# Kernel tuning notes

Hardware: AMD Instinct MI355X
Metric: run time of the kernel (lower is better)

## Reference

```python
import jax, jax.numpy as jnp
import numpy as np

L = 40   # seq_length (sentence includes root; sent_length = L-1)
B = 16   # batch
V = 10000  # vocab
F = 512  # feature_size = 2*hidden (bidirectional)
H = 256  # classifier hidden
NEG = -jnp.inf


def _mlp(x, W1, b1, W2, b2):
    # Classifier / BinaryClassifier: Linear -> tanh -> Linear
    return jnp.tanh(x @ W1 + b1) @ W2 + b2


def setup_inputs() -> dict:
    key = jax.random.key(0)
    ks = jax.random.split(key, 10)
    s = 0.05
    return {
        "h": jax.random.normal(ks[0], (L, B, F), jnp.float32),
        "sentence": jax.random.randint(ks[1], (L, B), 0, V),
        "Wt1": jax.random.normal(ks[2], (2 * F, H), jnp.float32) * s,
        "bt1": jnp.zeros((H,), jnp.float32),
        "Wt2": jax.random.normal(ks[3], (H, 1), jnp.float32) * s,
        "bt2": jnp.zeros((1,), jnp.float32),
        "Ww1": jax.random.normal(ks[4], (2 * F, H), jnp.float32) * s,
        "bw1": jnp.zeros((H,), jnp.float32),
        "Ww2": jax.random.normal(ks[5], (H, V), jnp.float32) * s,
        "bw2": jnp.zeros((V,), jnp.float32),
    }


def reference(h, sentence, Wt1, bt1, Wt2, bt2, Ww1, bw1, Ww2, bw2):
    sent_length = L - 1
    # all ordered pairs i < j (forward enumeration order of batch_feature_selection)
    iu, ju = np.triu_indices(L, k=1)          # [P]
    feat = jnp.concatenate([h[iu], h[ju]], axis=-1)   # [P, B, 2F]

    t_logit = _mlp(feat, Wt1, bt1, Wt2, bt2)[..., 0]  # [P, B]
    sh = jax.nn.log_sigmoid(-t_logit)                 # shift log-prob
    re = jax.nn.log_sigmoid(t_logit)                  # reduce log-prob

    # word model log-softmax, gathered at target token sentence[j+1]
    wl = _mlp(feat, Ww1, bw1, Ww2, bw2)               # [P, B, V]
    ju1 = np.minimum(ju + 1, L - 1)                   # pairs with j = L-1 are unused
    tgt = sentence[ju1]                               # [P, B]
    gathered = jnp.take_along_axis(wl, tgt[..., None], axis=-1)[..., 0]
    wlp = gathered - jax.nn.logsumexp(wl, axis=-1)    # [P, B]

    # dense [L, L, B] tables (only i<j entries used)
    SHW = jnp.full((L, L, B), NEG, jnp.float32).at[iu, ju].set(sh + wlp)  # word_prob_list
    RE = jnp.full((L, L, B), NEG, jnp.float32).at[iu, ju].set(re)

    # init cell: stack_next=False -> word prob of sentence[1] from features (0,0)
    feat0 = jnp.concatenate([h[0], h[0]], axis=-1)    # [B, 2F]
    lp0 = jax.nn.log_softmax(_mlp(feat0, Ww1, bw1, Ww2, bw2), axis=-1)
    init = jnp.take_along_axis(lp0, sentence[1][:, None], axis=1)[:, 0]  # [B]

    T = jnp.full((L, L, B), NEG, jnp.float32)
    T = T.at[0, 1].set(init)
    T = T.at[jnp.arange(1, sent_length), jnp.arange(2, sent_length + 1)].set(0.0)

    # CKY-style DP over span widths; each width is vectorized over start i and split k
    for gap in range(2, sent_length + 1):
        n_i = sent_length + 1 - gap
        i_arr = np.arange(n_i)
        j_arr = i_arr + gap
        k = i_arr[:, None] + np.arange(1, gap)[None, :]   # [n_i, gap-1]
        scores = (T[i_arr[:, None], k] + T[k, j_arr[:, None]]
                  + SHW[i_arr[:, None], k] + RE[k, j_arr[:, None]])  # [n_i, gap-1, B]
        T = T.at[i_arr, j_arr].set(jax.nn.logsumexp(scores, axis=1))

    # stack_next=False -> final_score = 0
    return T[0, sent_length]
```

## Files before the change

### kernel.cpp

```cpp
#include <hip/hip_runtime.h>
#include <hip/hip_bf16.h>

#define L_SEQ 40
#define B_SZ  16
#define V_SZ  10000
#define V_PAD 10240
#define NPAIR 780
#define NROWP 784
#define M_ROWS (NROWP * B_SZ)

typedef __attribute__((ext_vector_type(4))) float f32x4;
typedef __attribute__((ext_vector_type(4))) int   i32x4;
typedef __attribute__((ext_vector_type(8))) int   i32x8;

#if __has_builtin(__builtin_amdgcn_cvt_pk_fp8_f32)
__device__ __forceinline__ unsigned int pack4_fp8(float x0, float x1, float x2, float x3) {
    int lo = __builtin_amdgcn_cvt_pk_fp8_f32(x0, x1, 0, false);
    int full = __builtin_amdgcn_cvt_pk_fp8_f32(x2, x3, lo, true);
    return (unsigned int)full;
}
#else
__device__ __forceinline__ unsigned char f2e4m3(float f) {
    unsigned u = __float_as_uint(f);
    unsigned s = (u >> 24) & 0x80u;
    if ((u & 0x7FFFFFFFu) == 0) return (unsigned char)s;
    int E = (int)((u >> 23) & 0xFF) - 127 + 7;
    unsigned m = u & 0x7FFFFFu;
    if (E >= 16) return (unsigned char)(s | 0x7E);
    if (E >= 1) {
        unsigned keep = m >> 20, rest = m & 0xFFFFFu;
        keep += (rest > 0x80000u) || (rest == 0x80000u && (keep & 1));
        if (keep == 8) { keep = 0; E++; if (E >= 16) return (unsigned char)(s | 0x7E); }
        return (unsigned char)(s | (E << 3) | keep);
    }
    int shift = 1 - E;
    if (shift > 10) return (unsigned char)s;
    unsigned full = 0x800000u | m;
    unsigned sh = 20 + shift;
    unsigned keep = full >> sh, rem = full & ((1u << sh) - 1), half = 1u << (sh - 1);
    keep += (rem > half) || (rem == half && (keep & 1));
    if (keep >= 8) return (unsigned char)(s | (1 << 3));
    return (unsigned char)(s | keep);
}
__device__ __forceinline__ unsigned int pack4_fp8(float x0, float x1, float x2, float x3) {
    return (unsigned int)f2e4m3(x0) | ((unsigned int)f2e4m3(x1) << 8)
         | ((unsigned int)f2e4m3(x2) << 16) | ((unsigned int)f2e4m3(x3) << 24);
}
#endif

#if __has_builtin(__builtin_amdgcn_exp2f)
__device__ __forceinline__ float exp2_hw(float x) { return __builtin_amdgcn_exp2f(x); }
#else
__device__ __forceinline__ float exp2_hw(float x) { return __expf(x * 0.6931471805599453f); }
#endif

#if __has_builtin(__builtin_amdgcn_rcpf)
__device__ __forceinline__ float rcp_hw(float x) { return __builtin_amdgcn_rcpf(x); }
#else
__device__ __forceinline__ float rcp_hw(float x) { return 1.0f / x; }
#endif

__device__ __forceinline__ float fast_tanh(float x) {
    float e = exp2_hw(x * 2.885390081777926814f);
    return fmaf(-2.0f, rcp_hw(e + 1.0f), 1.0f);
}


__global__ __launch_bounds__(256) void prep_kernel(
        const float* __restrict__ Ww2, float* __restrict__ WwT,
        unsigned char* __restrict__ WbT,
        const float* __restrict__ h, const float* __restrict__ Wt1,
        const float* __restrict__ Ww1, float* __restrict__ UV) {
    const int bx = blockIdx.x;
    const int t = threadIdx.x;
    __shared__ float smem[32 * 132];
    if (bx < 640) {
        float (*tile)[132] = (float (*)[132])smem;
        int v0 = (bx % 80) * 128;
        int k0 = (bx / 80) * 32;
        int tx4 = t & 31, ky = t >> 5;
        int v = v0 + tx4 * 4;
#pragma unroll
        for (int r = 0; r < 4; r++) {
            int k = k0 + ky + r * 8;
            float4 val = make_float4(0.f, 0.f, 0.f, 0.f);
            if (v < V_SZ) val = *(const float4*)(Ww2 + (size_t)k * V_SZ + v);
            *(float4*)(&tile[ky + r * 8][tx4 * 4]) = val;
        }
        __syncthreads();
        int kx4 = t & 7, vr8 = t >> 3;
#pragma unroll
        for (int pass = 0; pass < 4; pass++) {
            int vr = vr8 + pass * 32;
            float c0 = tile[kx4 * 4 + 0][vr];
            float c1 = tile[kx4 * 4 + 1][vr];
            float c2 = tile[kx4 * 4 + 2][vr];
            float c3 = tile[kx4 * 4 + 3][vr];
            float4 cv = make_float4(c0, c1, c2, c3);
            *(float4*)(WwT + (size_t)(v0 + vr) * 256 + k0 + kx4 * 4) = cv;
            ((unsigned int*)WbT)[(size_t)(v0 + vr) * 64 + (k0 >> 2) + kx4] =
                pack4_fp8(c0, c1, c2, c3);
        }
    } else {
        float* hs = smem;
        int ub = bx - 640;
        int which = ub / 80;
        int m0 = (ub % 80) * 8;
        const float4* src = (const float4*)(h + (size_t)m0 * 512);
        float4* dst4 = (float4*)hs;
#pragma unroll
        for (int v = 0; v < 4; v++) dst4[v * 256 + t] = src[v * 256 + t];
        __syncthreads();
        const float* W = ((which < 2) ? Wt1 : Ww1) + ((which & 1) ? 512 * 256 : 0);
        float acc[8] = {};
        for (int f = 0; f < 512; f += 4) {
            float w0 = W[(f + 0) * 256 + t];
            float w1 = W[(f + 1) * 256 + t];
            float w2 = W[(f + 2) * 256 + t];
            float w3 = W[(f + 3) * 256 + t];
#pragma unroll
            for (int r = 0; r < 8; r++) {
                float4 hv = *(const float4*)(hs + r * 512 + f);
                acc[r] += hv.x * w0 + hv.y * w1 + hv.z * w2 + hv.w * w3;
            }
        }
        float* dst = UV + ((size_t)which * 640 + m0) * 256;
#pragma unroll
        for (int r = 0; r < 8; r++) dst[r * 256 + t] = acc[r];
    }
}

__global__ void build_rows(const float* __restrict__ UV,
                           const int* __restrict__ sentence,
                           const float* __restrict__ bt1,
                           const float* __restrict__ bw1,
                           const float* __restrict__ Wt2,
                           const float* __restrict__ bt2,
                           const float* __restrict__ WwT,
                           const float* __restrict__ bw2,
                           unsigned char* __restrict__ X,
                           float* __restrict__ tlog,
                           float* __restrict__ glog) {
    int w = blockIdx.x * 4 + (threadIdx.x >> 6);
    int lane = threadIdx.x & 63;
    int p = w >> 4, b = w & 15;
    int i = 0, j = 0;
    if (p < NPAIR) {
        int rem = p, len = L_SEQ - 1;
        while (rem >= len) { rem -= len; len--; i++; }
        j = i + 1 + rem;
    }
    int j1 = (j + 1 < L_SEQ) ? j + 1 : L_SEQ - 1;
    int tgt = sentence[j1 * B_SZ + b];
    const float4 ut = ((const float4*)(UV + 0 * 640 * 256 + (i * B_SZ + b) * 256))[lane];
    const float4 vt = ((const float4*)(UV + 1 * 640 * 256 + (j * B_SZ + b) * 256))[lane];
    const float4 uw = ((const float4*)(UV + 2 * 640 * 256 + (i * B_SZ + b) * 256))[lane];
    const float4 vw = ((const float4*)(UV + 3 * 640 * 256 + (j * B_SZ + b) * 256))[lane];
    const float4 bt = ((const float4*)bt1)[lane];
    const float4 bw = ((const float4*)bw1)[lane];
    const float4 w2 = ((const float4*)Wt2)[lane];
    const float4 wc = ((const float4*)(WwT + (size_t)tgt * 256))[lane];
    float xt0 = fast_tanh(ut.x + vt.x + bt.x), xt1 = fast_tanh(ut.y + vt.y + bt.y);
    float xt2 = fast_tanh(ut.z + vt.z + bt.z), xt3 = fast_tanh(ut.w + vt.w + bt.w);
    float xw0 = fast_tanh(uw.x + vw.x + bw.x), xw1 = fast_tanh(uw.y + vw.y + bw.y);
    float xw2 = fast_tanh(uw.z + vw.z + bw.z), xw3 = fast_tanh(uw.w + vw.w + bw.w);
    ((unsigned int*)X)[w * 64 + lane] = pack4_fp8(xw0, xw1, xw2, xw3);
    float td = xt0 * w2.x + xt1 * w2.y + xt2 * w2.z + xt3 * w2.w;
    float gd = xw0 * wc.x + xw1 * wc.y + xw2 * wc.z + xw3 * wc.w;
#pragma unroll
    for (int off = 32; off >= 1; off >>= 1) {
        td += __shfl_xor(td, off);
        gd += __shfl_xor(gd, off);
    }
    if (lane == 0) {
        tlog[w] = td + bt2[0];
        glog[w] = gd + bw2[tgt];
    }
}

#define RDQ(BASE, Q, BR) \
    BR[0] = *(const i32x4*)((BASE) + offs[(Q)*4+0]); \
    BR[1] = *(const i32x4*)((BASE) + offs[(Q)*4+1]); \
    BR[2] = *(const i32x4*)((BASE) + offs[(Q)*4+2]); \
    BR[3] = *(const i32x4*)((BASE) + offs[(Q)*4+3]);

#define MFQ(Q, BR) { \
    i32x8 bv0_ = __builtin_shufflevector(BR[0], BR[1], 0,1,2,3,4,5,6,7); \
    acc[0][((Q)&1)*2] = __builtin_amdgcn_mfma_scale_f32_16x16x128_f8f6f4( \
        apan[0][(Q)>>1], bv0_, acc[0][((Q)&1)*2], 0,0, 0,0x7F7F7F7F, 0,0x7F7F7F7F); \
    acc[1][((Q)&1)*2] = __builtin_amdgcn_mfma_scale_f32_16x16x128_f8f6f4( \
        apan[1][(Q)>>1], bv0_, acc[1][((Q)&1)*2], 0,0, 0,0x7F7F7F7F, 0,0x7F7F7F7F); \
    i32x8 bv1_ = __builtin_shufflevector(BR[2], BR[3], 0,1,2,3,4,5,6,7); \
    acc[0][((Q)&1)*2+1] = __builtin_amdgcn_mfma_scale_f32_16x16x128_f8f6f4( \
        apan[0][(Q)>>1], bv1_, acc[0][((Q)&1)*2+1], 0,0, 0,0x7F7F7F7F, 0,0x7F7F7F7F); \
    acc[1][((Q)&1)*2+1] = __builtin_amdgcn_mfma_scale_f32_16x16x128_f8f6f4( \
        apan[1][(Q)>>1], bv1_, acc[1][((Q)&1)*2+1], 0,0, 0,0x7F7F7F7F, 0,0x7F7F7F7F); \
}

__global__ __launch_bounds__(512, 2) void big_gemm(
        const unsigned char* __restrict__ X,
        const unsigned char* __restrict__ WbT,
        const float* __restrict__ bw2,
        float* __restrict__ rowsum) {
    __shared__ unsigned char Bs[3][64 * 256];
    __shared__ float biasL[2048];
    const int t = threadIdx.x;
    const int wid = t >> 6, lane = t & 63;
    const int l15 = lane & 15, l4 = lane >> 4;
    const int g = blockIdx.x;
    const int row0 = blockIdx.y * 256 + wid * 32;
    const int NIT = 32;
    const float L2E = 1.44269504088896340736f;

#pragma unroll
    for (int k = 0; k < 4; k++) {
        int idx = k * 512 + t;
        int col = g * 2048 + idx;
        biasL[idx] = (col < V_SZ) ? bw2[col] * L2E : -__builtin_inff();
    }

    int offs[16];
#pragma unroll
    for (int q = 0; q < 4; q++) {
        int kb = q >> 1, np = q & 1;
#pragma unroll
        for (int nn = 0; nn < 2; nn++)
#pragma unroll
            for (int gg = 0; gg < 2; gg++) {
                int ni = np * 2 + nn;
                int cc = ni * 16 + l15;
                int gr = kb * 8 + l4 * 2 + gg;
                offs[q * 4 + nn * 2 + gg] = cc * 256 + ((gr ^ (cc & 15)) << 4);
            }
    }

    auto dmaB = [&](int buf, int it) {
        const unsigned char* Bg = WbT + (size_t)(g * 2048 + it * 64) * 256;
#pragma unroll
        for (int q = 0; q < 2; q++) {
            int off = (wid * 2 + q) * 1024;
            int F = off + lane * 16;
            int cc = F >> 8;
            int s = (F >> 4) & 15;
            int srcg = s ^ (cc & 15);
            __builtin_amdgcn_global_load_lds(
                (const __attribute__((address_space(1))) unsigned int*)(Bg + cc * 256 + (srcg << 4)),
                (__attribute__((address_space(3))) unsigned int*)(&Bs[buf][0] + off),
                16, 0, 0);
        }
    };

    dmaB(0, 0);
    i32x8 apan[2][2];
    {
        const unsigned char* Ag = X + (size_t)row0 * 256;
#pragma unroll
        for (int mi = 0; mi < 2; mi++)
#pragma unroll
            for (int kb = 0; kb < 2; kb++)
                apan[mi][kb] = *(const i32x8*)(Ag + (mi * 16 + l15) * 256 + kb * 128 + l4 * 32);
    }
    dmaB(1, 1);
    __syncthreads();

    i32x4 br0[4], br1[4];
    RDQ(&Bs[0][0], 0, br0);

    float PS[2][4] = {};
    int bc = 0, bp = 2;

#pragma unroll 1
    for (int it = 0; it < NIT; it++) {
        asm volatile("s_waitcnt vmcnt(0)" ::: "memory");
        __builtin_amdgcn_s_barrier();
        if (it + 2 < NIT) dmaB(bp, it + 2);
        const unsigned char* bufC = &Bs[bc][0];
        int bn = (bc == 2) ? 0 : bc + 1;
        const unsigned char* bufN = &Bs[bn][0];
        float bl[4];
#pragma unroll
        for (int ni = 0; ni < 4; ni++) bl[ni] = biasL[it * 64 + ni * 16 + l15];
        f32x4 acc[2][4] = {};
        __builtin_amdgcn_s_setprio(1);
        RDQ(bufC, 1, br1); MFQ(0, br0);
        RDQ(bufC, 2, br0); MFQ(1, br1);
        RDQ(bufC, 3, br1); MFQ(2, br0);
        if (it + 1 < NIT) { RDQ(bufN, 0, br0); }
        MFQ(3, br1);
        __builtin_amdgcn_s_setprio(0);
#pragma unroll
        for (int ni = 0; ni < 4; ni++) {
            float bL = bl[ni];
#pragma unroll
            for (int mi = 0; mi < 2; mi++)
#pragma unroll
                for (int r = 0; r < 4; r++)
                    PS[mi][r] += exp2_hw(fmaf(acc[mi][ni][r], L2E, bL));
        }
        bc = bn;
        bp = (bp == 2) ? 0 : bp + 1;
    }
#pragma unroll
    for (int mi = 0; mi < 2; mi++)
#pragma unroll
        for (int r = 0; r < 4; r++) {
            float v = PS[mi][r];
            v += __shfl_xor(v, 1); v += __shfl_xor(v, 2);
            v += __shfl_xor(v, 4); v += __shfl_xor(v, 8);
            if (l15 == 0)
                atomicAdd(&rowsum[row0 + mi * 16 + l4 * 4 + r], v);
        }
}

__global__ __launch_bounds__(1024) void dp_kernel(const float* __restrict__ tlog,
                          const float* __restrict__ glog,
                          const float* __restrict__ rowsum,
                          float* __restrict__ out) {
    __shared__ float Tl[1600], SHWl[1600], REl[1600];
    const int t = threadIdx.x;
    const int b = blockIdx.x;
    const float NEGINF = -__builtin_inff();
    for (int idx = t; idx < 1600; idx += 1024) {
        Tl[idx] = NEGINF; SHWl[idx] = NEGINF; REl[idx] = NEGINF;
    }
    __syncthreads();
    for (int p = t; p < NPAIR; p += 1024) {
        int i = 0, rem = p, len = L_SEQ - 1;
        while (rem >= len) { rem -= len; len--; i++; }
        int j = i + 1 + rem;
        int row = p * 16 + b;
        float tl = tlog[row];
        float re_v = (tl >= 0.f) ? -log1pf(__expf(-tl)) : (tl - log1pf(__expf(tl)));
        float sh_v = (tl <= 0.f) ? -log1pf(__expf(tl)) : (-tl - log1pf(__expf(-tl)));
        float wlp = glog[row] - __logf(rowsum[row]);
        SHWl[i * 40 + j] = sh_v + wlp;
        REl[i * 40 + j] = re_v;
    }
    if (t == 0) {
        int row = NPAIR * 16 + b;
        Tl[0 * 40 + 1] = glog[row] - __logf(rowsum[row]);
    }
    if (t >= 1 && t <= 38) Tl[t * 40 + t + 1] = 0.f;
    __syncthreads();
    const int tg = t >> 4, li = t & 15;
    for (int gap = 2; gap <= L_SEQ - 1; gap++) {
        int n_i = L_SEQ - gap;
        float m = NEGINF, s = 0.f;
        int i = tg, j = tg + gap;
        if (tg < n_i) {
            for (int k = i + 1 + li; k < j; k += 16) {
                float v = Tl[i * 40 + k] + Tl[k * 40 + j]
                        + SHWl[i * 40 + k] + REl[k * 40 + j];
                if (v > m) { s = s * __expf(m - v) + 1.f; m = v; }
                else s += __expf(v - m);
            }
        }
#pragma unroll
        for (int off = 1; off < 16; off <<= 1) {
            float mo = __shfl_xor(m, off), so = __shfl_xor(s, off);
            float M = fmaxf(m, mo);
            float sn = 0.f;
            if (m > NEGINF) sn += s * __expf(m - M);
            if (mo > NEGINF) sn += so * __expf(mo - M);
            m = M; s = sn;
        }
        if (tg < n_i && li == 0) Tl[i * 40 + j] = m + __logf(s);
        __syncthreads();
    }
    if (t == 0) out[b] = Tl[39];
}

extern "C" void kernel_launch(void* const* d_in, const int* in_sizes, int n_in,
                              void* d_out, int out_size, void* d_ws, size_t ws_size,
                              hipStream_t stream) {
    const float* h        = (const float*)d_in[0];
    const int*   sentence = (const int*)d_in[1];
    const float* Wt1      = (const float*)d_in[2];
    const float* bt1      = (const float*)d_in[3];
    const float* Wt2      = (const float*)d_in[4];
    const float* bt2      = (const float*)d_in[5];
    const float* Ww1      = (const float*)d_in[6];
    const float* bw1      = (const float*)d_in[7];
    const float* Ww2      = (const float*)d_in[8];
    const float* bw2      = (const float*)d_in[9];
    float* out = (float*)d_out;

    char* ws = (char*)d_ws;
    size_t off = 0;
    float* UV = (float*)(ws + off);                    off += 4ull * 640 * 256 * 4;
    unsigned char* X = (unsigned char*)(ws + off);     off += (size_t)M_ROWS * 256;
    unsigned char* WbT = (unsigned char*)(ws + off);   off += (size_t)V_PAD * 256;
    float* WwT = (float*)(ws + off);                   off += (size_t)V_PAD * 256 * 4;
    float* rowsum = (float*)(ws + off);                off += (size_t)M_ROWS * 4;
    float* tlog = (float*)(ws + off);                  off += (size_t)M_ROWS * 4;
    float* glog = (float*)(ws + off);                  off += (size_t)M_ROWS * 4;

    hipMemsetAsync(rowsum, 0, (size_t)M_ROWS * 4, stream);
    prep_kernel<<<960, 256, 0, stream>>>(Ww2, WwT, WbT, h, Wt1, Ww1, UV);
    build_rows<<<M_ROWS / 4, 256, 0, stream>>>(UV, sentence, bt1, bw1, Wt2, bt2,
                                               WwT, bw2, X, tlog, glog);
    big_gemm<<<dim3(5, 49), 512, 0, stream>>>(X, WbT, bw2, rowsum);
    dp_kernel<<<16, 1024, 0, stream>>>(tlog, glog, rowsum, out);
}
```

Baseline: 198.9 us.

## Retile big_gemm warps to 64x64 tiles with 128-column B stages and interleaved epilogue

Each warp now computes a 64-row by 64-column tile: warp pairs share 64 rows and split a 128-column stage, instead of each warp covering 32 rows by 64 columns. Each B fragment loaded from LDS is therefore reused across four A panels, which halves LDS reads per MFMA, and the number of stages drops from 32 to 16. The exp2 epilogue is interleaved with the remaining MFMAs to overlap the transcendental work with matrix math, and cross-iteration B prefetch from LDS is dropped. In exchange, LDS use doubles (96KB for B buffers) and accumulator and A-panel register pressure rises, which may limit occupancy under the 2-block launch bound.

```diff
diff --git a/kernel.cpp b/kernel.cpp
--- a/kernel.cpp
+++ b/kernel.cpp
@@ -178,23 +178,35 @@
     }
 }
 
-#define RDQ(BASE, Q, BR) \
-    BR[0] = *(const i32x4*)((BASE) + offs[(Q)*4+0]); \
-    BR[1] = *(const i32x4*)((BASE) + offs[(Q)*4+1]); \
-    BR[2] = *(const i32x4*)((BASE) + offs[(Q)*4+2]); \
-    BR[3] = *(const i32x4*)((BASE) + offs[(Q)*4+3]);
-
-#define MFQ(Q, BR) { \
-    i32x8 bv0_ = __builtin_shufflevector(BR[0], BR[1], 0,1,2,3,4,5,6,7); \
-    acc[0][((Q)&1)*2] = __builtin_amdgcn_mfma_scale_f32_16x16x128_f8f6f4( \
-        apan[0][(Q)>>1], bv0_, acc[0][((Q)&1)*2], 0,0, 0,0x7F7F7F7F, 0,0x7F7F7F7F); \
-    acc[1][((Q)&1)*2] = __builtin_amdgcn_mfma_scale_f32_16x16x128_f8f6f4( \
-        apan[1][(Q)>>1], bv0_, acc[1][((Q)&1)*2], 0,0, 0,0x7F7F7F7F, 0,0x7F7F7F7F); \
-    i32x8 bv1_ = __builtin_shufflevector(BR[2], BR[3], 0,1,2,3,4,5,6,7); \
-    acc[0][((Q)&1)*2+1] = __builtin_amdgcn_mfma_scale_f32_16x16x128_f8f6f4( \
-        apan[0][(Q)>>1], bv1_, acc[0][((Q)&1)*2+1], 0,0, 0,0x7F7F7F7F, 0,0x7F7F7F7F); \
-    acc[1][((Q)&1)*2+1] = __builtin_amdgcn_mfma_scale_f32_16x16x128_f8f6f4( \
-        apan[1][(Q)>>1], bv1_, acc[1][((Q)&1)*2+1], 0,0, 0,0x7F7F7F7F, 0,0x7F7F7F7F); \
+#define RD8(BASE, KB, BR) \
+    BR[0] = *(const i32x4*)((BASE) + offs[(KB)*8 + 0]); \
+    BR[1] = *(const i32x4*)((BASE) + offs[(KB)*8 + 1]); \
+    BR[2] = *(const i32x4*)((BASE) + offs[(KB)*8 + 2]); \
+    BR[3] = *(const i32x4*)((BASE) + offs[(KB)*8 + 3]); \
+    BR[4] = *(const i32x4*)((BASE) + offs[(KB)*8 + 4]); \
+    BR[5] = *(const i32x4*)((BASE) + offs[(KB)*8 + 5]); \
+    BR[6] = *(const i32x4*)((BASE) + offs[(KB)*8 + 6]); \
+    BR[7] = *(const i32x4*)((BASE) + offs[(KB)*8 + 7]);
+
+#define MF4(KB, NI, BR) { \
+    i32x8 bv_ = __builtin_shufflevector(BR[2*(NI)], BR[2*(NI)+1], 0,1,2,3,4,5,6,7); \
+    acc[0][NI] = __builtin_amdgcn_mfma_scale_f32_16x16x128_f8f6f4( \
+        apan[0][KB], bv_, acc[0][NI], 0,0, 0,0x7F7F7F7F, 0,0x7F7F7F7F); \
+    acc[1][NI] = __builtin_amdgcn_mfma_scale_f32_16x16x128_f8f6f4( \
+        apan[1][KB], bv_, acc[1][NI], 0,0, 0,0x7F7F7F7F, 0,0x7F7F7F7F); \
+    acc[2][NI] = __builtin_amdgcn_mfma_scale_f32_16x16x128_f8f6f4( \
+        apan[2][KB], bv_, acc[2][NI], 0,0, 0,0x7F7F7F7F, 0,0x7F7F7F7F); \
+    acc[3][NI] = __builtin_amdgcn_mfma_scale_f32_16x16x128_f8f6f4( \
+        apan[3][KB], bv_, acc[3][NI], 0,0, 0,0x7F7F7F7F, 0,0x7F7F7F7F); \
+}
+
+#define EPI(NI) { \
+    float bL_ = bl[NI]; \
+    _Pragma("unroll") \
+    for (int mi_ = 0; mi_ < 4; mi_++) \
+        _Pragma("unroll") \
+        for (int r_ = 0; r_ < 4; r_++) \
+            PS[mi_][r_] += exp2_hw(fmaf(acc[mi_][NI][r_], L2E, bL_)); \
 }
 
 __global__ __launch_bounds__(512, 2) void big_gemm(
@@ -202,14 +214,15 @@
         const unsigned char* __restrict__ WbT,
         const float* __restrict__ bw2,
         float* __restrict__ rowsum) {
-    __shared__ unsigned char Bs[3][64 * 256];
+    __shared__ unsigned char Bs[3][128 * 256];
     __shared__ float biasL[2048];
     const int t = threadIdx.x;
     const int wid = t >> 6, lane = t & 63;
     const int l15 = lane & 15, l4 = lane >> 4;
+    const int rg = wid >> 1, ch = wid & 1;
     const int g = blockIdx.x;
-    const int row0 = blockIdx.y * 256 + wid * 32;
-    const int NIT = 32;
+    const int row0 = blockIdx.y * 256 + rg * 64;
+    const int NIT = 16;
     const float L2E = 1.44269504088896340736f;
 
 #pragma unroll
@@ -221,24 +234,21 @@
 
     int offs[16];
 #pragma unroll
-    for (int q = 0; q < 4; q++) {
-        int kb = q >> 1, np = q & 1;
-#pragma unroll
-        for (int nn = 0; nn < 2; nn++)
+    for (int kb = 0; kb < 2; kb++)
+#pragma unroll
+        for (int ni = 0; ni < 4; ni++)
 #pragma unroll
             for (int gg = 0; gg < 2; gg++) {
-                int ni = np * 2 + nn;
-                int cc = ni * 16 + l15;
+                int cc = ch * 64 + ni * 16 + l15;
                 int gr = kb * 8 + l4 * 2 + gg;
-                offs[q * 4 + nn * 2 + gg] = cc * 256 + ((gr ^ (cc & 15)) << 4);
+                offs[kb * 8 + ni * 2 + gg] = cc * 256 + ((gr ^ (cc & 15)) << 4);
             }
-    }
 
     auto dmaB = [&](int buf, int it) {
-        const unsigned char* Bg = WbT + (size_t)(g * 2048 + it * 64) * 256;
-#pragma unroll
-        for (int q = 0; q < 2; q++) {
-            int off = (wid * 2 + q) * 1024;
+        const unsigned char* Bg = WbT + (size_t)(g * 2048 + it * 128) * 256;
+#pragma unroll
+        for (int q = 0; q < 4; q++) {
+            int off = (wid * 4 + q) * 1024;
             int F = off + lane * 16;
             int cc = F >> 8;
             int s = (F >> 4) & 15;
@@ -251,11 +261,11 @@
     };
 
     dmaB(0, 0);
-    i32x8 apan[2][2];
+    i32x8 apan[4][2];
     {
         const unsigned char* Ag = X + (size_t)row0 * 256;
 #pragma unroll
-        for (int mi = 0; mi < 2; mi++)
+        for (int mi = 0; mi < 4; mi++)
 #pragma unroll
             for (int kb = 0; kb < 2; kb++)
                 apan[mi][kb] = *(const i32x8*)(Ag + (mi * 16 + l15) * 256 + kb * 128 + l4 * 32);
@@ -263,10 +273,7 @@
     dmaB(1, 1);
     __syncthreads();
 
-    i32x4 br0[4], br1[4];
-    RDQ(&Bs[0][0], 0, br0);
-
-    float PS[2][4] = {};
+    float PS[4][4] = {};
     int bc = 0, bp = 2;
 
 #pragma unroll 1
@@ -275,33 +282,27 @@
         __builtin_amdgcn_s_barrier();
         if (it + 2 < NIT) dmaB(bp, it + 2);
         const unsigned char* bufC = &Bs[bc][0];
-        int bn = (bc == 2) ? 0 : bc + 1;
-        const unsigned char* bufN = &Bs[bn][0];
         float bl[4];
 #pragma unroll
-        for (int ni = 0; ni < 4; ni++) bl[ni] = biasL[it * 64 + ni * 16 + l15];
-        f32x4 acc[2][4] = {};
+        for (int ni = 0; ni < 4; ni++)
+            bl[ni] = biasL[it * 128 + ch * 64 + ni * 16 + l15];
+        f32x4 acc[4][4] = {};
+        i32x4 br[8];
         __builtin_amdgcn_s_setprio(1);
-        RDQ(bufC, 1, br1); MFQ(0, br0);
-        RDQ(bufC, 2, br0); MFQ(1, br1);
-        RDQ(bufC, 3, br1); MFQ(2, br0);
-        if (it + 1 < NIT) { RDQ(bufN, 0, br0); }
-        MFQ(3, br1);
+        RD8(bufC, 0, br);
+        MF4(0, 0, br); MF4(0, 1, br); MF4(0, 2, br); MF4(0, 3, br);
+        RD8(bufC, 1, br);
+        MF4(1, 0, br);
+        MF4(1, 1, br); EPI(0);
+        MF4(1, 2, br); EPI(1);
+        MF4(1, 3, br); EPI(2);
         __builtin_amdgcn_s_setprio(0);
-#pragma unroll
-        for (int ni = 0; ni < 4; ni++) {
-            float bL = bl[ni];
-#pragma unroll
-            for (int mi = 0; mi < 2; mi++)
-#pragma unroll
-                for (int r = 0; r < 4; r++)
-                    PS[mi][r] += exp2_hw(fmaf(acc[mi][ni][r], L2E, bL));
-        }
-        bc = bn;
+        EPI(3);
+        bc = (bc == 2) ? 0 : bc + 1;
         bp = (bp == 2) ? 0 : bp + 1;
     }
 #pragma unroll
-    for (int mi = 0; mi < 2; mi++)
+    for (int mi = 0; mi < 4; mi++)
 #pragma unroll
         for (int r = 0; r < 4; r++) {
             float v = PS[mi][r];
```

Measured after the change: 193.5 us. -2.7%, faster.

## Split-K the UV projection and retile big_gemm into smaller double-buffered blocks

Applied to the files above, without the earlier changes.

The UV projection part of prep_kernel is split four ways along the feature dimension. Each block accumulates its partial result with atomicAdd into a UV buffer that is zeroed beforehand, which doubles the prep grid. big_gemm moves from 512-thread blocks with a 3-stage buffer and 2048 columns to 256-thread blocks with 1280 columns, 128 rows and a 2-stage buffer. That raises its grid from 245 to 784 blocks for better CU coverage, at the cost of less B reuse per block, no cross-iteration register prefetch, and extra atomics plus a memset.

```diff
diff --git a/kernel.cpp b/kernel.cpp
--- a/kernel.cpp
+++ b/kernel.cpp
@@ -104,29 +104,34 @@
     } else {
         float* hs = smem;
         int ub = bx - 640;
-        int which = ub / 80;
-        int m0 = (ub % 80) * 8;
-        const float4* src = (const float4*)(h + (size_t)m0 * 512);
-        float4* dst4 = (float4*)hs;
-#pragma unroll
-        for (int v = 0; v < 4; v++) dst4[v * 256 + t] = src[v * 256 + t];
+        int which = ub / 320;
+        int rem = ub - which * 320;
+        int m0 = (rem >> 2) * 8;
+        int ks = rem & 3;
+        int f0 = ks * 128;
+        {
+            int r = t >> 5, fq = t & 31;
+            ((float4*)hs)[r * 32 + fq] =
+                *(const float4*)(h + (size_t)(m0 + r) * 512 + f0 + fq * 4);
+        }
         __syncthreads();
-        const float* W = ((which < 2) ? Wt1 : Ww1) + ((which & 1) ? 512 * 256 : 0);
+        const float* W = ((which < 2) ? Wt1 : Ww1)
+                       + ((which & 1) ? 512 * 256 : 0) + (size_t)f0 * 256;
         float acc[8] = {};
-        for (int f = 0; f < 512; f += 4) {
+        for (int f = 0; f < 128; f += 4) {
             float w0 = W[(f + 0) * 256 + t];
             float w1 = W[(f + 1) * 256 + t];
             float w2 = W[(f + 2) * 256 + t];
             float w3 = W[(f + 3) * 256 + t];
 #pragma unroll
             for (int r = 0; r < 8; r++) {
-                float4 hv = *(const float4*)(hs + r * 512 + f);
+                float4 hv = *(const float4*)(hs + r * 128 + f);
                 acc[r] += hv.x * w0 + hv.y * w1 + hv.z * w2 + hv.w * w3;
             }
         }
         float* dst = UV + ((size_t)which * 640 + m0) * 256;
 #pragma unroll
-        for (int r = 0; r < 8; r++) dst[r * 256 + t] = acc[r];
+        for (int r = 0; r < 8; r++) atomicAdd(&dst[r * 256 + t], acc[r]);
     }
 }
 
@@ -197,25 +202,25 @@
         apan[1][(Q)>>1], bv1_, acc[1][((Q)&1)*2+1], 0,0, 0,0x7F7F7F7F, 0,0x7F7F7F7F); \
 }
 
-__global__ __launch_bounds__(512, 2) void big_gemm(
+__global__ __launch_bounds__(256, 4) void big_gemm(
         const unsigned char* __restrict__ X,
         const unsigned char* __restrict__ WbT,
         const float* __restrict__ bw2,
         float* __restrict__ rowsum) {
-    __shared__ unsigned char Bs[3][64 * 256];
-    __shared__ float biasL[2048];
+    __shared__ unsigned char Bs[2][64 * 256];
+    __shared__ float biasL[1280];
     const int t = threadIdx.x;
     const int wid = t >> 6, lane = t & 63;
     const int l15 = lane & 15, l4 = lane >> 4;
     const int g = blockIdx.x;
-    const int row0 = blockIdx.y * 256 + wid * 32;
-    const int NIT = 32;
+    const int row0 = blockIdx.y * 128 + wid * 32;
+    const int NIT = 20;
     const float L2E = 1.44269504088896340736f;
 
 #pragma unroll
-    for (int k = 0; k < 4; k++) {
-        int idx = k * 512 + t;
-        int col = g * 2048 + idx;
+    for (int k = 0; k < 5; k++) {
+        int idx = k * 256 + t;
+        int col = g * 1280 + idx;
         biasL[idx] = (col < V_SZ) ? bw2[col] * L2E : -__builtin_inff();
     }
 
@@ -235,10 +240,10 @@
     }
 
     auto dmaB = [&](int buf, int it) {
-        const unsigned char* Bg = WbT + (size_t)(g * 2048 + it * 64) * 256;
-#pragma unroll
-        for (int q = 0; q < 2; q++) {
-            int off = (wid * 2 + q) * 1024;
+        const unsigned char* Bg = WbT + (size_t)(g * 1280 + it * 64) * 256;
+#pragma unroll
+        for (int q = 0; q < 4; q++) {
+            int off = (wid * 4 + q) * 1024;
             int F = off + lane * 16;
             int cc = F >> 8;
             int s = (F >> 4) & 15;
@@ -260,32 +265,26 @@
             for (int kb = 0; kb < 2; kb++)
                 apan[mi][kb] = *(const i32x8*)(Ag + (mi * 16 + l15) * 256 + kb * 128 + l4 * 32);
     }
-    dmaB(1, 1);
     __syncthreads();
 
-    i32x4 br0[4], br1[4];
-    RDQ(&Bs[0][0], 0, br0);
-
     float PS[2][4] = {};
-    int bc = 0, bp = 2;
 
 #pragma unroll 1
     for (int it = 0; it < NIT; it++) {
         asm volatile("s_waitcnt vmcnt(0)" ::: "memory");
         __builtin_amdgcn_s_barrier();
-        if (it + 2 < NIT) dmaB(bp, it + 2);
-        const unsigned char* bufC = &Bs[bc][0];
-        int bn = (bc == 2) ? 0 : bc + 1;
-        const unsigned char* bufN = &Bs[bn][0];
+        if (it + 1 < NIT) dmaB((it + 1) & 1, it + 1);
+        const unsigned char* bufC = &Bs[it & 1][0];
         float bl[4];
 #pragma unroll
         for (int ni = 0; ni < 4; ni++) bl[ni] = biasL[it * 64 + ni * 16 + l15];
         f32x4 acc[2][4] = {};
+        i32x4 br0[4], br1[4];
         __builtin_amdgcn_s_setprio(1);
+        RDQ(bufC, 0, br0);
         RDQ(bufC, 1, br1); MFQ(0, br0);
         RDQ(bufC, 2, br0); MFQ(1, br1);
         RDQ(bufC, 3, br1); MFQ(2, br0);
-        if (it + 1 < NIT) { RDQ(bufN, 0, br0); }
         MFQ(3, br1);
         __builtin_amdgcn_s_setprio(0);
 #pragma unroll
@@ -297,8 +296,6 @@
                 for (int r = 0; r < 4; r++)
                     PS[mi][r] += exp2_hw(fmaf(acc[mi][ni][r], L2E, bL));
         }
-        bc = bn;
-        bp = (bp == 2) ? 0 : bp + 1;
     }
 #pragma unroll
     for (int mi = 0; mi < 2; mi++)
@@ -396,9 +393,10 @@
     float* glog = (float*)(ws + off);                  off += (size_t)M_ROWS * 4;
 
     hipMemsetAsync(rowsum, 0, (size_t)M_ROWS * 4, stream);
-    prep_kernel<<<960, 256, 0, stream>>>(Ww2, WwT, WbT, h, Wt1, Ww1, UV);
+    hipMemsetAsync(UV, 0, 4ull * 640 * 256 * 4, stream);
+    prep_kernel<<<1920, 256, 0, stream>>>(Ww2, WwT, WbT, h, Wt1, Ww1, UV);
     build_rows<<<M_ROWS / 4, 256, 0, stream>>>(UV, sentence, bt1, bw1, Wt2, bt2,
                                                WwT, bw2, X, tlog, glog);
-    big_gemm<<<dim3(5, 49), 512, 0, stream>>>(X, WbT, bw2, rowsum);
+    big_gemm<<<dim3(8, 98), 256, 0, stream>>>(X, WbT, bw2, rowsum);
     dp_kernel<<<16, 1024, 0, stream>>>(tlog, glog, rowsum, out);
 }
```

Result: faster. 185.4 us (-6.8%).
